# Kernel optimization log

Measured on AMD Instinct MI355X. Metric: run time of the kernel, lower is better.

The kernel has to match this reference:

```python
import jax, jax.numpy as jnp
import numpy as np

B, T, H = 16, 4096, 512


def setup_inputs() -> dict:
    key = jax.random.key(0)
    k1, k2, k3 = jax.random.split(key, 3)
    inputs = jax.random.normal(k1, (B, T, H), dtype=jnp.float32)
    # lengths in [1, T] so the global mean pool is well-defined
    lengths = jax.random.randint(k2, (B,), 1, T + 1, dtype=jnp.int32)
    mask = jax.random.randint(k3, (B, T), 0, 2).astype(bool)
    return {"inputs": inputs, "lengths": lengths, "mask": mask}


def _mean_pool(x, lengths):
    # length-masked mean pool: [B, T, H] -> [B, H]
    t = x.shape[1]
    valid = (jnp.arange(t)[None, :] < lengths[:, None]).astype(x.dtype)  # [B, T]
    summed = jnp.einsum('bth,bt->bh', x, valid)
    denom = jnp.maximum(lengths, 1).astype(x.dtype)[:, None]
    return summed / denom


def _span_select(x, mask):
    # Compact masked tokens to the front of each row (stable order), zero the tail.
    # Equivalent to the TF while_loop + scatter_nd/gather_nd compaction:
    # stable argsort of ~mask puts True positions first, in original order.
    order = jnp.argsort(jnp.logical_not(mask), axis=1, stable=True)  # [B, T]
    dense = jnp.take_along_axis(x, order[:, :, None], axis=1)        # [B, T, H]
    span_lengths = jnp.sum(mask.astype(jnp.int32), axis=1)           # [B]
    dense_mask = jnp.arange(x.shape[1])[None, :] < span_lengths[:, None]
    dense = dense * dense_mask[:, :, None].astype(x.dtype)
    return dense, span_lengths


def reference(inputs, lengths, mask):
    global_view = _mean_pool(inputs, lengths)            # [B, H]
    spans, span_lengths = _span_select(inputs, mask)     # [B, T, H], [B]
    local_view = _mean_pool(spans, span_lengths)         # [B, H]
    return jnp.concatenate([global_view, local_view], axis=-1)  # [B, 2H]
```

## Files before the change

kernel.cpp:

```cpp
#include <hip/hip_runtime.h>


constexpr int Bc = 16;
constexpr int Tc = 4096;
constexpr int Hc = 512;
constexpr int H4 = Hc / 4;
constexpr int CHUNK   = 16;
constexpr int NCHUNK  = Tc / CHUNK;
constexpr int NBLK    = Bc * NCHUNK;
constexpr int NROW    = NBLK * 2;
constexpr int ROWS_PB = NROW / Bc;
constexpr int G2      = 8;
constexpr int R2ROWS  = ROWS_PB / G2;

__global__ __launch_bounds__(256) void glp_partial(
    const float* __restrict__ x,
    const int* __restrict__ lengths,
    const int* __restrict__ mask,
    float* __restrict__ pg,
    float* __restrict__ pl,
    int*   __restrict__ pcnt)
{
    const int blk  = blockIdx.x;
    const int b    = blk >> 8;
    const int c    = blk & (NCHUNK - 1);
    const int t0   = c * CHUNK;
    const int lane = threadIdx.x & 127;
    const int par  = threadIdx.x >> 7;
    const int len  = lengths[b];

    const float4* __restrict__ xb =
        (const float4*)x + ((size_t)b * Tc + t0 + par) * H4 + lane;
    const int* __restrict__ mb = mask + (size_t)b * Tc + t0 + par;

    float4 v[8]; int m[8];
    #pragma unroll
    for (int j = 0; j < 8; ++j) {
        v[j] = xb[(size_t)(2 * j) * H4];
        m[j] = mb[2 * j];
    }

    float4 g = make_float4(0.f, 0.f, 0.f, 0.f);
    float4 l = make_float4(0.f, 0.f, 0.f, 0.f);
    int mc = 0;
    #pragma unroll
    for (int j = 0; j < 8; ++j) {
        const float wg = (t0 + par + 2 * j < len) ? 1.f : 0.f;
        const float wl = m[j] ? 1.f : 0.f;
        g.x = fmaf(v[j].x, wg, g.x); g.y = fmaf(v[j].y, wg, g.y);
        g.z = fmaf(v[j].z, wg, g.z); g.w = fmaf(v[j].w, wg, g.w);
        l.x = fmaf(v[j].x, wl, l.x); l.y = fmaf(v[j].y, wl, l.y);
        l.z = fmaf(v[j].z, wl, l.z); l.w = fmaf(v[j].w, wl, l.w);
        mc += (m[j] != 0);
    }

    const int row = blk * 2 + par;
    ((float4*)(pg + (size_t)row * Hc))[lane] = g;
    ((float4*)(pl + (size_t)row * Hc))[lane] = l;
    if (lane == 0) pcnt[row] = mc;
}

__global__ __launch_bounds__(128) void glp_reduce1(
    const float* __restrict__ pg, const float* __restrict__ pl,
    const int* __restrict__ pcnt,
    float* __restrict__ qg, float* __restrict__ ql, int* __restrict__ qcnt)
{
    const int blk  = blockIdx.x;
    const int r0   = blk * R2ROWS;
    const int lane = threadIdx.x;
    const float4* pg4 = (const float4*)pg + (size_t)r0 * H4 + lane;
    const float4* pl4 = (const float4*)pl + (size_t)r0 * H4 + lane;

    float4 gs = make_float4(0.f, 0.f, 0.f, 0.f);
    float4 ls = make_float4(0.f, 0.f, 0.f, 0.f);
    for (int r = 0; r < R2ROWS; r += 8) {
        float4 a[8], d[8];
        #pragma unroll
        for (int j = 0; j < 8; ++j) {
            a[j] = pg4[(size_t)(r + j) * H4];
            d[j] = pl4[(size_t)(r + j) * H4];
        }
        #pragma unroll
        for (int j = 0; j < 8; ++j) {
            gs.x += a[j].x; gs.y += a[j].y; gs.z += a[j].z; gs.w += a[j].w;
            ls.x += d[j].x; ls.y += d[j].y; ls.z += d[j].z; ls.w += d[j].w;
        }
    }
    ((float4*)(qg + (size_t)blk * Hc))[lane] = gs;
    ((float4*)(ql + (size_t)blk * Hc))[lane] = ls;
    if (lane == 0) {
        int mc = 0;
        for (int r = 0; r < R2ROWS; ++r) mc += pcnt[r0 + r];
        qcnt[blk] = mc;
    }
}

__global__ __launch_bounds__(128) void glp_reduce2(
    const float* __restrict__ qg, const float* __restrict__ ql,
    const int* __restrict__ qcnt, const int* __restrict__ lengths,
    float* __restrict__ out)
{
    const int b    = blockIdx.x;
    const int lane = threadIdx.x;
    float4 gs = make_float4(0.f, 0.f, 0.f, 0.f);
    float4 ls = make_float4(0.f, 0.f, 0.f, 0.f);
    #pragma unroll
    for (int k = 0; k < G2; ++k) {
        float4 a = ((const float4*)(qg + (size_t)(b * G2 + k) * Hc))[lane];
        float4 d = ((const float4*)(ql + (size_t)(b * G2 + k) * Hc))[lane];
        gs.x += a.x; gs.y += a.y; gs.z += a.z; gs.w += a.w;
        ls.x += d.x; ls.y += d.y; ls.z += d.z; ls.w += d.w;
    }
    int cnt = 0;
    #pragma unroll
    for (int k = 0; k < G2; ++k) cnt += qcnt[b * G2 + k];
    const float invl = 1.f / (float)max(lengths[b], 1);
    const float invc = 1.f / (float)max(cnt, 1);
    gs.x *= invl; gs.y *= invl; gs.z *= invl; gs.w *= invl;
    ls.x *= invc; ls.y *= invc; ls.z *= invc; ls.w *= invc;
    ((float4*)(out + (size_t)b * 2 * Hc))[lane]      = gs;
    ((float4*)(out + (size_t)b * 2 * Hc + Hc))[lane] = ls;
}

__global__ __launch_bounds__(128) void glp_partial_atomic(
    const float* __restrict__ x, const int* __restrict__ lengths,
    const int* __restrict__ mask,
    float* __restrict__ gsum, float* __restrict__ lsum, int* __restrict__ cnt)
{
    const int blk  = blockIdx.x;
    const int b    = blk >> 6;
    const int c    = blk & 63;
    const int t0   = c * 64;
    const int lane = threadIdx.x;
    const int len  = lengths[b];
    const float4* __restrict__ xb =
        (const float4*)x + ((size_t)b * Tc + t0) * H4 + lane;
    const int* __restrict__ mb = mask + (size_t)b * Tc + t0;

    float4 g = make_float4(0.f, 0.f, 0.f, 0.f);
    float4 l = make_float4(0.f, 0.f, 0.f, 0.f);
    int mc = 0;
    for (int ii = 0; ii < 64; ii += 8) {
        float4 v[8]; int m[8];
        #pragma unroll
        for (int j = 0; j < 8; ++j) { v[j] = xb[(size_t)(ii + j) * H4]; m[j] = mb[ii + j]; }
        #pragma unroll
        for (int j = 0; j < 8; ++j) {
            const float wg = (t0 + ii + j < len) ? 1.f : 0.f;
            const float wl = m[j] ? 1.f : 0.f;
            g.x = fmaf(v[j].x, wg, g.x); g.y = fmaf(v[j].y, wg, g.y);
            g.z = fmaf(v[j].z, wg, g.z); g.w = fmaf(v[j].w, wg, g.w);
            l.x = fmaf(v[j].x, wl, l.x); l.y = fmaf(v[j].y, wl, l.y);
            l.z = fmaf(v[j].z, wl, l.z); l.w = fmaf(v[j].w, wl, l.w);
            mc += (m[j] != 0);
        }
    }
    float* gp = gsum + b * Hc + lane * 4;
    float* lp = lsum + b * Hc + lane * 4;
    atomicAdd(gp + 0, g.x); atomicAdd(gp + 1, g.y);
    atomicAdd(gp + 2, g.z); atomicAdd(gp + 3, g.w);
    atomicAdd(lp + 0, l.x); atomicAdd(lp + 1, l.y);
    atomicAdd(lp + 2, l.z); atomicAdd(lp + 3, l.w);
    if (lane == 0) atomicAdd(cnt + b, mc);
}

__global__ __launch_bounds__(512) void glp_finalize(
    const float* __restrict__ gsum, const float* __restrict__ lsum,
    const int* __restrict__ cnt, const int* __restrict__ lengths,
    float* __restrict__ out)
{
    const int b = blockIdx.x;
    const int h = threadIdx.x;
    out[b * 2 * Hc + h]      = gsum[b * Hc + h] / (float)max(lengths[b], 1);
    out[b * 2 * Hc + Hc + h] = lsum[b * Hc + h] / (float)max(cnt[b], 1);
}

extern "C" void kernel_launch(void* const* d_in, const int* in_sizes, int n_in,
                              void* d_out, int out_size, void* d_ws, size_t ws_size,
                              hipStream_t stream) {
    const float* x     = (const float*)d_in[0];
    const int* lengths = (const int*)d_in[1];
    const int* mask    = (const int*)d_in[2];
    float* out = (float*)d_out;

    const size_t npg   = (size_t)NROW * Hc;
    const size_t nq    = (size_t)Bc * G2 * Hc;
    const size_t need  = (2 * npg + 2 * nq) * sizeof(float)
                       + (NROW + Bc * G2) * sizeof(int);
    if (ws_size >= need) {
        float* pg   = (float*)d_ws;
        float* pl   = pg + npg;
        float* qg   = pl + npg;
        float* ql   = qg + nq;
        int*   pcnt = (int*)(ql + nq);
        int*   qcnt = pcnt + NROW;
        glp_partial<<<NBLK, 256, 0, stream>>>(x, lengths, mask, pg, pl, pcnt);
        glp_reduce1<<<Bc * G2, 128, 0, stream>>>(pg, pl, pcnt, qg, ql, qcnt);
        glp_reduce2<<<Bc, 128, 0, stream>>>(qg, ql, qcnt, lengths, out);
    } else {
        float* gsum = (float*)d_ws;
        float* lsum = gsum + Bc * Hc;
        int*   cnt  = (int*)(lsum + Bc * Hc);
        const size_t zb = (size_t)(2 * Bc * Hc) * sizeof(float) + Bc * sizeof(int);
        hipMemsetAsync(d_ws, 0, zb, stream);
        glp_partial_atomic<<<Bc * 64, 128, 0, stream>>>(x, lengths, mask, gsum, lsum, cnt);
        glp_finalize<<<Bc, Hc, 0, stream>>>(gsum, lsum, cnt, lengths, out);
    }
}
```

Measured before the change: 204.1 us.

## Cut partial-sum traffic with larger per-block chunks and single reduce pass

Each partial block now covers 32 tokens strided by 256 instead of 16 contiguous tokens, and its two thread halves combine their sums in shared memory, so it writes one partial row instead of two. That shrinks the partial buffers from 8192 rows to 2048. The two reduction kernels become one, which splits columns across 8 blocks per batch and does a shared-memory tree step. The aim is less global round-trip traffic and one fewer launch, at the cost of a strided token access pattern and fewer partial blocks in flight.

```diff
diff --git a/kernel.cpp b/kernel.cpp
--- a/kernel.cpp
+++ b/kernel.cpp
@@ -5,13 +5,10 @@
 constexpr int Tc = 4096;
 constexpr int Hc = 512;
 constexpr int H4 = Hc / 4;
-constexpr int CHUNK   = 16;
-constexpr int NCHUNK  = Tc / CHUNK;
-constexpr int NBLK    = Bc * NCHUNK;
-constexpr int NROW    = NBLK * 2;
-constexpr int ROWS_PB = NROW / Bc;
-constexpr int G2      = 8;
-constexpr int R2ROWS  = ROWS_PB / G2;
+constexpr int CPB    = 128;
+constexpr int NBLK   = Bc * CPB;
+constexpr int ROWS_PB = CPB;
+constexpr int KITER  = 16;
 
 __global__ __launch_bounds__(256) void glp_partial(
     const float* __restrict__ x,
@@ -22,104 +19,112 @@
     int*   __restrict__ pcnt)
 {
     const int blk  = blockIdx.x;
-    const int b    = blk >> 8;
-    const int c    = blk & (NCHUNK - 1);
-    const int t0   = c * CHUNK;
+    const int b    = blk >> 7;
+    const int c    = blk & (CPB - 1);
     const int lane = threadIdx.x & 127;
-    const int par  = threadIdx.x >> 7;
+    const int par  = __builtin_amdgcn_readfirstlane(threadIdx.x >> 7);
+    const int tbase = 2 * c + par;
     const int len  = lengths[b];
 
     const float4* __restrict__ xb =
-        (const float4*)x + ((size_t)b * Tc + t0 + par) * H4 + lane;
-    const int* __restrict__ mb = mask + (size_t)b * Tc + t0 + par;
-
-    float4 v[8]; int m[8];
-    #pragma unroll
-    for (int j = 0; j < 8; ++j) {
-        v[j] = xb[(size_t)(2 * j) * H4];
-        m[j] = mb[2 * j];
-    }
+        (const float4*)x + ((size_t)b * Tc + tbase) * H4 + lane;
+    const int* __restrict__ mrow = mask + (size_t)b * Tc + tbase;
 
     float4 g = make_float4(0.f, 0.f, 0.f, 0.f);
     float4 l = make_float4(0.f, 0.f, 0.f, 0.f);
     int mc = 0;
+
     #pragma unroll
-    for (int j = 0; j < 8; ++j) {
-        const float wg = (t0 + par + 2 * j < len) ? 1.f : 0.f;
-        const float wl = m[j] ? 1.f : 0.f;
-        g.x = fmaf(v[j].x, wg, g.x); g.y = fmaf(v[j].y, wg, g.y);
-        g.z = fmaf(v[j].z, wg, g.z); g.w = fmaf(v[j].w, wg, g.w);
-        l.x = fmaf(v[j].x, wl, l.x); l.y = fmaf(v[j].y, wl, l.y);
-        l.z = fmaf(v[j].z, wl, l.z); l.w = fmaf(v[j].w, wl, l.w);
-        mc += (m[j] != 0);
-    }
-
-    const int row = blk * 2 + par;
-    ((float4*)(pg + (size_t)row * Hc))[lane] = g;
-    ((float4*)(pl + (size_t)row * Hc))[lane] = l;
-    if (lane == 0) pcnt[row] = mc;
-}
-
-__global__ __launch_bounds__(128) void glp_reduce1(
+    for (int half = 0; half < 2; ++half) {
+        float4 v[8]; int m[8];
+        #pragma unroll
+        for (int j = 0; j < 8; ++j) {
+            const int k = half * 8 + j;
+            v[j] = xb[(size_t)k * 256 * H4];
+            m[j] = mrow[k * 256];
+        }
+        #pragma unroll
+        for (int j = 0; j < 8; ++j) {
+            const int k = half * 8 + j;
+            const int t = tbase + 256 * k;
+            const float wg = (t < len) ? 1.f : 0.f;
+            const float wl = m[j] ? 1.f : 0.f;
+            g.x = fmaf(v[j].x, wg, g.x); g.y = fmaf(v[j].y, wg, g.y);
+            g.z = fmaf(v[j].z, wg, g.z); g.w = fmaf(v[j].w, wg, g.w);
+            l.x = fmaf(v[j].x, wl, l.x); l.y = fmaf(v[j].y, wl, l.y);
+            l.z = fmaf(v[j].z, wl, l.z); l.w = fmaf(v[j].w, wl, l.w);
+            mc += (m[j] != 0);
+        }
+    }
+
+    __shared__ float4 sg[128];
+    __shared__ float4 sl[128];
+    __shared__ int smc[2];
+    if (par == 1) { sg[lane] = g; sl[lane] = l; }
+    if (threadIdx.x == 0)   smc[0] = mc;
+    if (threadIdx.x == 128) smc[1] = mc;
+    __syncthreads();
+    if (par == 0) {
+        const float4 og = sg[lane], ol = sl[lane];
+        g.x += og.x; g.y += og.y; g.z += og.z; g.w += og.w;
+        l.x += ol.x; l.y += ol.y; l.z += ol.z; l.w += ol.w;
+        ((float4*)(pg + (size_t)blk * Hc))[lane] = g;
+        ((float4*)(pl + (size_t)blk * Hc))[lane] = l;
+    }
+    if (threadIdx.x == 0) pcnt[blk] = smc[0] + smc[1];
+}
+
+__global__ __launch_bounds__(128) void glp_reduce(
     const float* __restrict__ pg, const float* __restrict__ pl,
-    const int* __restrict__ pcnt,
-    float* __restrict__ qg, float* __restrict__ ql, int* __restrict__ qcnt)
-{
-    const int blk  = blockIdx.x;
-    const int r0   = blk * R2ROWS;
-    const int lane = threadIdx.x;
-    const float4* pg4 = (const float4*)pg + (size_t)r0 * H4 + lane;
-    const float4* pl4 = (const float4*)pl + (size_t)r0 * H4 + lane;
-
-    float4 gs = make_float4(0.f, 0.f, 0.f, 0.f);
-    float4 ls = make_float4(0.f, 0.f, 0.f, 0.f);
-    for (int r = 0; r < R2ROWS; r += 8) {
-        float4 a[8], d[8];
-        #pragma unroll
-        for (int j = 0; j < 8; ++j) {
-            a[j] = pg4[(size_t)(r + j) * H4];
-            d[j] = pl4[(size_t)(r + j) * H4];
-        }
-        #pragma unroll
-        for (int j = 0; j < 8; ++j) {
-            gs.x += a[j].x; gs.y += a[j].y; gs.z += a[j].z; gs.w += a[j].w;
-            ls.x += d[j].x; ls.y += d[j].y; ls.z += d[j].z; ls.w += d[j].w;
-        }
-    }
-    ((float4*)(qg + (size_t)blk * Hc))[lane] = gs;
-    ((float4*)(ql + (size_t)blk * Hc))[lane] = ls;
-    if (lane == 0) {
-        int mc = 0;
-        for (int r = 0; r < R2ROWS; ++r) mc += pcnt[r0 + r];
-        qcnt[blk] = mc;
-    }
-}
-
-__global__ __launch_bounds__(128) void glp_reduce2(
-    const float* __restrict__ qg, const float* __restrict__ ql,
-    const int* __restrict__ qcnt, const int* __restrict__ lengths,
+    const int* __restrict__ pcnt, const int* __restrict__ lengths,
     float* __restrict__ out)
 {
-    const int b    = blockIdx.x;
-    const int lane = threadIdx.x;
+    const int b   = blockIdx.x >> 3;
+    const int o   = blockIdx.x & 7;
+    const int col = o * 16 + (threadIdx.x & 15);
+    const int rg  = threadIdx.x >> 4;
+
+    const float4* pg4 = (const float4*)pg;
+    const float4* pl4 = (const float4*)pl;
+
     float4 gs = make_float4(0.f, 0.f, 0.f, 0.f);
     float4 ls = make_float4(0.f, 0.f, 0.f, 0.f);
     #pragma unroll
-    for (int k = 0; k < G2; ++k) {
-        float4 a = ((const float4*)(qg + (size_t)(b * G2 + k) * Hc))[lane];
-        float4 d = ((const float4*)(ql + (size_t)(b * G2 + k) * Hc))[lane];
-        gs.x += a.x; gs.y += a.y; gs.z += a.z; gs.w += a.w;
-        ls.x += d.x; ls.y += d.y; ls.z += d.z; ls.w += d.w;
-    }
-    int cnt = 0;
-    #pragma unroll
-    for (int k = 0; k < G2; ++k) cnt += qcnt[b * G2 + k];
-    const float invl = 1.f / (float)max(lengths[b], 1);
-    const float invc = 1.f / (float)max(cnt, 1);
-    gs.x *= invl; gs.y *= invl; gs.z *= invl; gs.w *= invl;
-    ls.x *= invc; ls.y *= invc; ls.z *= invc; ls.w *= invc;
-    ((float4*)(out + (size_t)b * 2 * Hc))[lane]      = gs;
-    ((float4*)(out + (size_t)b * 2 * Hc + Hc))[lane] = ls;
+    for (int half = 0; half < 2; ++half) {
+        float4 a[8], d[8];
+        #pragma unroll
+        for (int j = 0; j < 8; ++j) {
+            const int r = b * ROWS_PB + rg + 8 * (half * 8 + j);
+            a[j] = pg4[(size_t)r * H4 + col];
+            d[j] = pl4[(size_t)r * H4 + col];
+        }
+        #pragma unroll
+        for (int j = 0; j < 8; ++j) {
+            gs.x += a[j].x; gs.y += a[j].y; gs.z += a[j].z; gs.w += a[j].w;
+            ls.x += d[j].x; ls.y += d[j].y; ls.z += d[j].z; ls.w += d[j].w;
+        }
+    }
+
+    __shared__ float4 lg[128], ll[128];
+    lg[threadIdx.x] = gs; ll[threadIdx.x] = ls;
+    __syncthreads();
+    if (rg == 0) {
+        #pragma unroll
+        for (int j = 1; j < 8; ++j) {
+            const float4 a = lg[j * 16 + (threadIdx.x & 15)];
+            const float4 d = ll[j * 16 + (threadIdx.x & 15)];
+            gs.x += a.x; gs.y += a.y; gs.z += a.z; gs.w += a.w;
+            ls.x += d.x; ls.y += d.y; ls.z += d.z; ls.w += d.w;
+        }
+        int cnt = 0;
+        for (int i = 0; i < ROWS_PB; ++i) cnt += pcnt[b * ROWS_PB + i];
+        const float invl = 1.f / (float)max(lengths[b], 1);
+        const float invc = 1.f / (float)max(cnt, 1);
+        gs.x *= invl; gs.y *= invl; gs.z *= invl; gs.w *= invl;
+        ls.x *= invc; ls.y *= invc; ls.z *= invc; ls.w *= invc;
+        ((float4*)out)[b * 256 + col]       = gs;
+        ((float4*)out)[b * 256 + 128 + col] = ls;
+    }
 }
 
 __global__ __launch_bounds__(128) void glp_partial_atomic(
@@ -183,20 +188,14 @@
     const int* mask    = (const int*)d_in[2];
     float* out = (float*)d_out;
 
-    const size_t npg   = (size_t)NROW * Hc;
-    const size_t nq    = (size_t)Bc * G2 * Hc;
-    const size_t need  = (2 * npg + 2 * nq) * sizeof(float)
-                       + (NROW + Bc * G2) * sizeof(int);
+    const size_t npg  = (size_t)NBLK * Hc;
+    const size_t need = 2 * npg * sizeof(float) + NBLK * sizeof(int);
     if (ws_size >= need) {
         float* pg   = (float*)d_ws;
         float* pl   = pg + npg;
-        float* qg   = pl + npg;
-        float* ql   = qg + nq;
-        int*   pcnt = (int*)(ql + nq);
-        int*   qcnt = pcnt + NROW;
+        int*   pcnt = (int*)(pl + npg);
         glp_partial<<<NBLK, 256, 0, stream>>>(x, lengths, mask, pg, pl, pcnt);
-        glp_reduce1<<<Bc * G2, 128, 0, stream>>>(pg, pl, pcnt, qg, ql, qcnt);
-        glp_reduce2<<<Bc, 128, 0, stream>>>(qg, ql, qcnt, lengths, out);
+        glp_reduce<<<Bc * 8, 128, 0, stream>>>(pg, pl, pcnt, lengths, out);
     } else {
         float* gsum = (float*)d_ws;
         float* lsum = gsum + Bc * Hc;
```

After: 193.8 us. 1.05x faster.
